# Kernel tuning notes

Hardware: AMD Instinct MI355X
Metric: run time of the kernel (lower is better)

Reference implementation:

```python
import jax, jax.numpy as jnp
import numpy as np

V = 50257; CTX = 2048; D = 1024; H = 16; L = 8; DH = D // H
B = 2; S = 2048; EPS = 1e-5


def setup_inputs() -> dict:
    key = jax.random.key(0)
    ks = jax.random.split(key, 8)
    s = 0.02
    def n(k, shape):
        return jax.random.normal(k, shape, jnp.float32) * s
    return {
        "x": jax.random.randint(ks[0], (B, S), 0, V),
        "wte": n(ks[1], (V, D)),
        "wpe": n(ks[2], (CTX, D)),
        "ln1_g": jnp.ones((L, D), jnp.float32), "ln1_b": jnp.zeros((L, D), jnp.float32),
        "w_qkv": n(ks[3], (L, D, 3 * D)), "b_qkv": jnp.zeros((L, 3 * D), jnp.float32),
        "w_proj": n(ks[4], (L, D, D)), "b_proj": jnp.zeros((L, D), jnp.float32),
        "ln2_g": jnp.ones((L, D), jnp.float32), "ln2_b": jnp.zeros((L, D), jnp.float32),
        "w_fc": n(ks[5], (L, D, 4 * D)), "b_fc": jnp.zeros((L, 4 * D), jnp.float32),
        "w_cp": n(ks[6], (L, 4 * D, D)), "b_cp": jnp.zeros((L, D), jnp.float32),
        "lnf_g": jnp.ones((D,), jnp.float32), "lnf_b": jnp.zeros((D,), jnp.float32),
        "w_head": n(ks[7], (D, V)),
    }


def layernorm(x, g, b):
    m = x.mean(-1, keepdims=True)
    v = ((x - m) ** 2).mean(-1, keepdims=True)
    return (x - m) * jax.lax.rsqrt(v + EPS) * g + b


def gpt_forward(x, wte, wpe, ln1_g, ln1_b, w_qkv, b_qkv, w_proj, b_proj,
                ln2_g, ln2_b, w_fc, b_fc, w_cp, b_cp, lnf_g, lnf_b, w_head):
    Bx, Sx = x.shape
    h = wte[x] + wpe[:Sx]                       # [B,S,D]
    mask = jnp.tril(jnp.ones((Sx, Sx), bool))   # causal mask
    scale = DH ** -0.5

    def block(h, p):
        g1, b1, wq, bq, wp, bp, g2, b2, wf, bf, wc, bc = p
        y = layernorm(h, g1, b1)
        qkv = y @ wq + bq                        # [B,S,3D]
        q, k, v = jnp.split(qkv, 3, axis=-1)
        q = q.reshape(Bx, Sx, H, DH)
        k = k.reshape(Bx, Sx, H, DH)
        v = v.reshape(Bx, Sx, H, DH)
        att = jnp.einsum('bqhd,bkhd->bhqk', q, k) * scale
        att = jnp.where(mask, att, -jnp.inf)
        att = jax.nn.softmax(att, axis=-1)
        z = jnp.einsum('bhqk,bkhd->bqhd', att, v).reshape(Bx, Sx, D)
        h = h + z @ wp + bp
        y2 = layernorm(h, g2, b2)
        h = h + jax.nn.gelu(y2 @ wf + bf, approximate=False) @ wc + bc
        return h, None

    h, _ = jax.lax.scan(block, h, (ln1_g, ln1_b, w_qkv, b_qkv, w_proj, b_proj,
                                   ln2_g, ln2_b, w_fc, b_fc, w_cp, b_cp))
    h = layernorm(h, lnf_g, lnf_b)
    logits = h[:, -1:, :] @ w_head              # [B,1,V] (last position only)
    return logits


def reference(x, wte, wpe, ln1_g, ln1_b, w_qkv, b_qkv, w_proj, b_proj,
              ln2_g, ln2_b, w_fc, b_fc, w_cp, b_cp, lnf_g, lnf_b, w_head):
    return gpt_forward(x, wte, wpe, ln1_g, ln1_b, w_qkv, b_qkv, w_proj, b_proj,
                       ln2_g, ln2_b, w_fc, b_fc, w_cp, b_cp, lnf_g, lnf_b, w_head)
```

## Files before the change

### kernel.cpp

```cpp
#include <hip/hip_runtime.h>
#include <hip/hip_bf16.h>
#include <math.h>

#define VOCAB 50257
#define CTX 2048
#define DMODEL 1024
#define NHEAD 16
#define NLAYER 8
#define DHEAD 64
#define BATCH 2
#define SEQ 2048
#define NTOK (BATCH * SEQ)

typedef __bf16 bf16x8 __attribute__((ext_vector_type(8)));
typedef float  f32x4  __attribute__((ext_vector_type(4)));
typedef unsigned short ushort4v __attribute__((ext_vector_type(4)));
typedef unsigned short ushort8v __attribute__((ext_vector_type(8)));

__device__ inline void gl_lds16(const void* g, void* l) {
    __builtin_amdgcn_global_load_lds(
        (const __attribute__((address_space(1))) unsigned int*)g,
        (__attribute__((address_space(3))) unsigned int*)l, 16, 0, 0);
}

__device__ inline unsigned short f2bs(float v) {
    __hip_bfloat16 t = __float2bfloat16(v);
    return *(unsigned short*)&t;
}

__global__ void embed_kernel(const int* __restrict__ x,
                             const float* __restrict__ wte,
                             const float* __restrict__ wpe,
                             float* __restrict__ h) {
    int t = blockIdx.x;
    int s = t & (SEQ - 1);
    int tok = x[t];
    const float* pe = wpe + (long)s * DMODEL;
    const float* te = wte + (long)tok * DMODEL;
    float* ph = h + (long)t * DMODEL;
    for (int d = threadIdx.x; d < DMODEL; d += 256)
        ph[d] = te[d] + pe[d];
}

__device__ inline float wave_sum(float v) {
    for (int off = 32; off; off >>= 1) v += __shfl_xor(v, off);
    return v;
}

__device__ void ln_body(char* smem, int row, const float* __restrict__ in,
                        unsigned short* __restrict__ out,
                        const float* __restrict__ g, const float* __restrict__ b) {
    float* red  = (float*)smem;
    float* red2 = red + 4;
    const float* px = in + (long)row * DMODEL;
    unsigned short* po = out + (long)row * DMODEL;
    int tid = threadIdx.x;
    int wid = tid >> 6, lane = tid & 63;

    float x[4];
    float s = 0.f;
    #pragma unroll
    for (int i = 0; i < 4; ++i) { x[i] = px[tid + i * 256]; s += x[i]; }
    s = wave_sum(s);
    if (lane == 0) red[wid] = s;
    __syncthreads();
    float mean = (red[0] + red[1] + red[2] + red[3]) * (1.0f / DMODEL);

    float s2 = 0.f;
    #pragma unroll
    for (int i = 0; i < 4; ++i) { float d = x[i] - mean; s2 += d * d; }
    s2 = wave_sum(s2);
    if (lane == 0) red2[wid] = s2;
    __syncthreads();
    float var = (red2[0] + red2[1] + red2[2] + red2[3]) * (1.0f / DMODEL);
    float r = 1.0f / sqrtf(var + 1e-5f);
    #pragma unroll
    for (int i = 0; i < 4; ++i) {
        int d = tid + i * 256;
        po[d] = f2bs((x[i] - mean) * r * g[d] + b[d]);
    }
}

__global__ void ln_final(const float* __restrict__ in, float* __restrict__ out,
                         const float* __restrict__ g, const float* __restrict__ b,
                         long row_stride) {
    __shared__ float red[4], red2[4];
    int row = blockIdx.x;
    const float* px = in + (long)row * row_stride;
    float* po = out + (long)row * DMODEL;
    int tid = threadIdx.x;
    int wid = tid >> 6, lane = tid & 63;
    float x[4];
    float s = 0.f;
    #pragma unroll
    for (int i = 0; i < 4; ++i) { x[i] = px[tid + i * 256]; s += x[i]; }
    s = wave_sum(s);
    if (lane == 0) red[wid] = s;
    __syncthreads();
    float mean = (red[0] + red[1] + red[2] + red[3]) * (1.0f / DMODEL);
    float s2 = 0.f;
    #pragma unroll
    for (int i = 0; i < 4; ++i) { float d = x[i] - mean; s2 += d * d; }
    s2 = wave_sum(s2);
    if (lane == 0) red2[wid] = s2;
    __syncthreads();
    float var = (red2[0] + red2[1] + red2[2] + red2[3]) * (1.0f / DMODEL);
    float r = 1.0f / sqrtf(var + 1e-5f);
    #pragma unroll
    for (int i = 0; i < 4; ++i) {
        int d = tid + i * 256;
        po[d] = (x[i] - mean) * r * g[d] + b[d];
    }
}

__device__ void convT_body(char* smem, int kx, int ny, const float* __restrict__ W,
                           unsigned short* __restrict__ WT, int K, int N) {
    float (*t)[65] = (float(*)[65])smem;
    const int k0 = kx * 64, n0 = ny * 64;
    const int tid = threadIdx.x;
    {
        const int krow = tid >> 4, c4 = (tid & 15) * 4;
        #pragma unroll
        for (int p = 0; p < 4; ++p) {
            f32x4 gv = *(const f32x4*)&W[(long)(k0 + p * 16 + krow) * N + n0 + c4];
            #pragma unroll
            for (int j = 0; j < 4; ++j) t[p * 16 + krow][c4 + j] = gv[j];
        }
    }
    __syncthreads();
    {
        const int n = tid >> 3, kl = (tid & 7) * 8;
        #pragma unroll
        for (int p = 0; p < 2; ++p) {
            ushort8v pk;
            #pragma unroll
            for (int j = 0; j < 8; ++j) pk[j] = f2bs(t[kl + j][p * 32 + n]);
            *(ushort8v*)&WT[(long)(n0 + p * 32 + n) * K + k0 + kl] = pk;
        }
    }
}

__global__ __launch_bounds__(256)
void mm_qkv(const unsigned short* __restrict__ A,
            const unsigned short* __restrict__ BT,
            const float* __restrict__ bias,
            unsigned short* __restrict__ qkvB, int M, int N, int K) {
    __shared__ unsigned short As[128 * 32];
    __shared__ unsigned short Bs[128 * 32];
    const int tid = threadIdx.x;
    const int w = tid >> 6, lane = tid & 63;
    const int bm = blockIdx.y * 128, bn = blockIdx.x * 128;
    const int wr = (w >> 1) * 64, wc = (w & 1) * 64;

    f32x4 acc[4][4];
    #pragma unroll
    for (int m = 0; m < 4; ++m)
        #pragma unroll
        for (int n = 0; n < 4; ++n)
            acc[m][n] = (f32x4){0.f, 0.f, 0.f, 0.f};

    const int lrow = lane >> 2;
    const int lcol = (lane & 3) * 8;
    const unsigned short* gA = A + (long)(bm + w * 32 + lrow) * K + lcol;
    const unsigned short* gB = BT + (long)(bn + w * 32 + lrow) * K + lcol;
    unsigned short* lA = &As[(w * 32) * 32];
    unsigned short* lB = &Bs[(w * 32) * 32];

    for (int k0 = 0; k0 < K; k0 += 32) {
        gl_lds16(gA + k0,          lA);
        gl_lds16(gA + k0 + 16 * K, lA + 16 * 32);
        gl_lds16(gB + k0,          lB);
        gl_lds16(gB + k0 + 16 * K, lB + 16 * 32);
        __syncthreads();

        bf16x8 a[4], b[4];
        #pragma unroll
        for (int m = 0; m < 4; ++m)
            a[m] = *(const bf16x8*)&As[(wr + m * 16 + (lane & 15)) * 32 + (lane >> 4) * 8];
        #pragma unroll
        for (int n = 0; n < 4; ++n)
            b[n] = *(const bf16x8*)&Bs[(wc + n * 16 + (lane & 15)) * 32 + (lane >> 4) * 8];
        #pragma unroll
        for (int m = 0; m < 4; ++m)
            #pragma unroll
            for (int n = 0; n < 4; ++n)
                acc[m][n] = __builtin_amdgcn_mfma_f32_16x16x32_bf16(a[m], b[n], acc[m][n], 0, 0, 0);
        __syncthreads();
    }

    const int r0 = (lane >> 4) * 4, cc = lane & 15;
    #pragma unroll
    for (int n = 0; n < 4; ++n) {
        int colb = bn + wc + n * 16;
        float bv = bias[colb + cc];
        #pragma unroll
        for (int m = 0; m < 4; ++m) {
            int rowb = bm + wr + m * 16 + r0;
            int which = colb >> 10, hh = (colb & 1023) >> 6, dbase = colb & 63;
            int b_ = rowb >> 11, s_ = rowb & 2047;
            long bh2 = b_ * 16 + hh;
            float v[4];
            #pragma unroll
            for (int r = 0; r < 4; ++r) v[r] = acc[m][n][r] + bv;
            if (which == 2) {
                ushort4v pk;
                #pragma unroll
                for (int r = 0; r < 4; ++r) pk[r] = f2bs(v[r]);
                *(ushort4v*)&qkvB[8388608L + (bh2 * 64 + dbase + cc) * 2048 + s_] = pk;
            } else {
                unsigned short* dst = qkvB + (long)which * 4194304L +
                                      (bh2 * 2048 + s_) * 64 + dbase + cc;
                #pragma unroll
                for (int r = 0; r < 4; ++r) dst[r * 64] = f2bs(v[r]);
            }
        }
    }
}

__device__ void mm128_gelu_body(char* smem, int bx, int by,
                                const unsigned short* __restrict__ A,
                                const unsigned short* __restrict__ BT,
                                const float* __restrict__ bias,
                                unsigned short* __restrict__ Cout, int M, int N, int K) {
    unsigned short* As = (unsigned short*)smem;
    unsigned short* Bs = As + 128 * 32;
    const int tid = threadIdx.x;
    const int w = tid >> 6, lane = tid & 63;
    const int bm = by * 128, bn = bx * 128;
    const int wr = (w >> 1) * 64, wc = (w & 1) * 64;

    f32x4 acc[4][4];
    #pragma unroll
    for (int m = 0; m < 4; ++m)
        #pragma unroll
        for (int n = 0; n < 4; ++n)
            acc[m][n] = (f32x4){0.f, 0.f, 0.f, 0.f};

    const int lrow = lane >> 2;
    const int lcol = (lane & 3) * 8;
    const unsigned short* gA = A + (long)(bm + w * 32 + lrow) * K + lcol;
    const unsigned short* gB = BT + (long)(bn + w * 32 + lrow) * K + lcol;
    unsigned short* lA = &As[(w * 32) * 32];
    unsigned short* lB = &Bs[(w * 32) * 32];

    for (int k0 = 0; k0 < K; k0 += 32) {
        gl_lds16(gA + k0,          lA);
        gl_lds16(gA + k0 + 16 * K, lA + 16 * 32);
        gl_lds16(gB + k0,          lB);
        gl_lds16(gB + k0 + 16 * K, lB + 16 * 32);
        __syncthreads();

        bf16x8 a[4], b[4];
        #pragma unroll
        for (int m = 0; m < 4; ++m)
            a[m] = *(const bf16x8*)&As[(wr + m * 16 + (lane & 15)) * 32 + (lane >> 4) * 8];
        #pragma unroll
        for (int n = 0; n < 4; ++n)
            b[n] = *(const bf16x8*)&Bs[(wc + n * 16 + (lane & 15)) * 32 + (lane >> 4) * 8];
        #pragma unroll
        for (int m = 0; m < 4; ++m)
            #pragma unroll
            for (int n = 0; n < 4; ++n)
                acc[m][n] = __builtin_amdgcn_mfma_f32_16x16x32_bf16(a[m], b[n], acc[m][n], 0, 0, 0);
        __syncthreads();
    }

    const int r0 = (lane >> 4) * 4, cc = lane & 15;
    #pragma unroll
    for (int n = 0; n < 4; ++n) {
        int colb = bn + wc + n * 16;
        float bv = bias[colb + cc];
        #pragma unroll
        for (int m = 0; m < 4; ++m) {
            int rowb = bm + wr + m * 16 + r0;
            #pragma unroll
            for (int r = 0; r < 4; ++r) {
                long row = rowb + r, col = colb + cc;
                float v = acc[m][n][r] + bv;
                v = 0.5f * v * (1.0f + erff(v * 0.70710678118f));
                Cout[row * N + col] = f2bs(v);
            }
        }
    }
}

__global__ __launch_bounds__(256)
void mm_mfma_n64(const unsigned short* __restrict__ A,
                 const unsigned short* __restrict__ BT,
                 const float* __restrict__ bias, const float* __restrict__ R,
                 float* __restrict__ Cout, int M, int N, int K) {
    __shared__ unsigned short As[128 * 32];
    __shared__ unsigned short Bs[64 * 32];
    const int tid = threadIdx.x;
    const int w = tid >> 6, lane = tid & 63;
    const int bm = blockIdx.y * 128, bn = blockIdx.x * 64;
    const int wr = (w >> 1) * 64, wc = (w & 1) * 32;

    f32x4 acc[4][2];
    #pragma unroll
    for (int m = 0; m < 4; ++m)
        #pragma unroll
        for (int n = 0; n < 2; ++n)
            acc[m][n] = (f32x4){0.f, 0.f, 0.f, 0.f};

    const int lrow = lane >> 2;
    const int lcol = (lane & 3) * 8;
    const unsigned short* gA = A + (long)(bm + w * 32 + lrow) * K + lcol;
    const unsigned short* gB = BT + (long)(bn + w * 16 + lrow) * K + lcol;
    unsigned short* lA = &As[(w * 32) * 32];
    unsigned short* lB = &Bs[(w * 16) * 32];

    for (int k0 = 0; k0 < K; k0 += 32) {
        gl_lds16(gA + k0,          lA);
        gl_lds16(gA + k0 + 16 * K, lA + 16 * 32);
        gl_lds16(gB + k0,          lB);
        __syncthreads();

        bf16x8 a[4], b[2];
        #pragma unroll
        for (int m = 0; m < 4; ++m)
            a[m] = *(const bf16x8*)&As[(wr + m * 16 + (lane & 15)) * 32 + (lane >> 4) * 8];
        #pragma unroll
        for (int n = 0; n < 2; ++n)
            b[n] = *(const bf16x8*)&Bs[(wc + n * 16 + (lane & 15)) * 32 + (lane >> 4) * 8];
        #pragma unroll
        for (int m = 0; m < 4; ++m)
            #pragma unroll
            for (int n = 0; n < 2; ++n)
                acc[m][n] = __builtin_amdgcn_mfma_f32_16x16x32_bf16(a[m], b[n], acc[m][n], 0, 0, 0);
        __syncthreads();
    }

    const int r0 = (lane >> 4) * 4, cc = lane & 15;
    #pragma unroll
    for (int n = 0; n < 2; ++n) {
        int colb = bn + wc + n * 16;
        float bv = bias[colb + cc];
        #pragma unroll
        for (int m = 0; m < 4; ++m) {
            int rowb = bm + wr + m * 16 + r0;
            #pragma unroll
            for (int r = 0; r < 4; ++r) {
                long row = rowb + r, col = colb + cc;
                float v = acc[m][n][r] + bv + R[row * N + col];
                Cout[row * N + col] = v;
            }
        }
    }
}

__device__ void attn_body(char* smem, int bh, int qb,
                          const unsigned short* __restrict__ qB,
                          const unsigned short* __restrict__ kB,
                          const unsigned short* __restrict__ vT,
                          __hip_bfloat16* __restrict__ z) {
    const int tid = threadIdx.x, w = tid >> 6, lane = tid & 63;
    const int arow = lane & 15, kg = lane >> 4;
    unsigned short* Ks = (unsigned short*)smem;
    unsigned short* Vs = Ks + 128 * 64;
    unsigned short* Ps = Vs + 64 * 128 + w * 16 * 128;

    const long kvbase = (long)bh * (2048 * 64);

    bf16x8 qa[2];
    {
        const unsigned short* q0 = qB + kvbase + (long)(qb + w * 16 + arow) * 64 + kg * 8;
        qa[0] = *(const bf16x8*)(q0);
        qa[1] = *(const bf16x8*)(q0 + 32);
    }

    f32x4 po[4];
    float mrow[4], lrow[4];
    #pragma unroll
    for (int i = 0; i < 4; ++i) {
        po[i] = (f32x4){0.f, 0.f, 0.f, 0.f};
        mrow[i] = -1e30f; lrow[i] = 0.f;
    }

    const int ksrow = lane >> 3;
    const int kschunk = (lane & 7) ^ ksrow;
    const int vsr = lane >> 4;
    const int cmax = qb >> 7;

    for (int c = 0; c <= cmax; ++c) {
        {
            const unsigned short* ks0 = kB + kvbase +
                (long)(c * 128 + w * 32 + ksrow) * 64 + kschunk * 8;
            #pragma unroll
            for (int i = 0; i < 4; ++i)
                gl_lds16(ks0 + (long)i * 8 * 64, &Ks[(w * 32 + i * 8) * 64]);
            #pragma unroll
            for (int i = 0; i < 4; ++i) {
                int d = w * 16 + i * 4 + vsr;
                int sch = (lane & 15) ^ (d & 7);
                gl_lds16(vT + kvbase + (long)d * 2048 + c * 128 + sch * 8,
                         &Vs[(w * 16 + i * 4) * 128]);
            }
        }
        __syncthreads();

        f32x4 s[8];
        #pragma unroll
        for (int n = 0; n < 8; ++n) {
            s[n] = (f32x4){0.f, 0.f, 0.f, 0.f};
            int row = n * 16 + arow, sw = row & 7;
            bf16x8 kb0 = *(const bf16x8*)&Ks[row * 64 + (kg ^ sw) * 8];
            bf16x8 kb1 = *(const bf16x8*)&Ks[row * 64 + ((4 + kg) ^ sw) * 8];
            s[n] = __builtin_amdgcn_mfma_f32_16x16x32_bf16(qa[0], kb0, s[n], 0, 0, 0);
            s[n] = __builtin_amdgcn_mfma_f32_16x16x32_bf16(qa[1], kb1, s[n], 0, 0, 0);
        }

        const bool diag = (c == cmax);
        #pragma unroll
        for (int n = 0; n < 8; ++n)
            #pragma unroll
            for (int r = 0; r < 4; ++r) {
                float v = s[n][r] * 0.125f;
                if (diag) {
                    int key = c * 128 + n * 16 + arow;
                    int qrow = qb + w * 16 + kg * 4 + r;
                    if (key > qrow) v = -1e30f;
                }
                s[n][r] = v;
            }

        #pragma unroll
        for (int r = 0; r < 4; ++r) {
            float rm = s[0][r];
            #pragma unroll
            for (int n = 1; n < 8; ++n) rm = fmaxf(rm, s[n][r]);
            #pragma unroll
            for (int off = 1; off < 16; off <<= 1)
                rm = fmaxf(rm, __shfl_xor(rm, off));
            float mnew = fmaxf(mrow[r], rm);
            float esc = expf(mrow[r] - mnew);
            float rs = 0.f;
            #pragma unroll
            for (int n = 0; n < 8; ++n) {
                float p = expf(s[n][r] - mnew);
                s[n][r] = p;
                rs += p;
            }
            #pragma unroll
            for (int off = 1; off < 16; off <<= 1)
                rs += __shfl_xor(rs, off);
            lrow[r] = lrow[r] * esc + rs;
            #pragma unroll
            for (int dt = 0; dt < 4; ++dt) po[dt][r] *= esc;
            mrow[r] = mnew;
        }

        #pragma unroll
        for (int n = 0; n < 8; ++n) {
            int col = n * 16 + arow;
            int chunk = col >> 3, cw = col & 7;
            #pragma unroll
            for (int r = 0; r < 4; ++r) {
                int row = kg * 4 + r;
                Ps[row * 128 + ((chunk ^ (row & 7)) * 8 + cw)] = f2bs(s[n][r]);
            }
        }

        bf16x8 pa[4];
        #pragma unroll
        for (int ks = 0; ks < 4; ++ks)
            pa[ks] = *(const bf16x8*)&Ps[arow * 128 + (((ks * 4 + kg) ^ (arow & 7)) * 8)];
        #pragma unroll
        for (int dt = 0; dt < 4; ++dt) {
            int vrow = dt * 16 + arow, sw = vrow & 7;
            #pragma unroll
            for (int ks = 0; ks < 4; ++ks) {
                bf16x8 vb = *(const bf16x8*)&Vs[vrow * 128 + (((ks * 4 + kg) ^ sw) * 8)];
                po[dt] = __builtin_amdgcn_mfma_f32_16x16x32_bf16(pa[ks], vb, po[dt], 0, 0, 0);
            }
        }
        __syncthreads();
    }

    const int b_ = bh >> 4, hofs = (bh & 15) * 64;
    #pragma unroll
    for (int dt = 0; dt < 4; ++dt)
        #pragma unroll
        for (int r = 0; r < 4; ++r) {
            long row = (long)b_ * 2048 + qb + w * 16 + kg * 4 + r;
            z[row * 1024 + hofs + dt * 16 + arow] = __float2bfloat16(po[dt][r] / lrow[r]);
        }
}

__global__ __launch_bounds__(256)
void fused_ln_convT(const float* __restrict__ h, unsigned short* __restrict__ y,
                    const float* __restrict__ g, const float* __restrict__ b,
                    const float* __restrict__ W, unsigned short* __restrict__ WT,
                    int K, int N, int nLN) {
    extern __shared__ char smem[];
    int bid = blockIdx.x;
    if (bid < nLN) {
        ln_body(smem, bid, h, y, g, b);
    } else {
        int r = bid - nLN, kt = K >> 6;
        convT_body(smem, r % kt, r / kt, W, WT, K, N);
    }
}

__global__ __launch_bounds__(256)
void fused_attn_convT(const unsigned short* __restrict__ qB,
                      const unsigned short* __restrict__ kB,
                      const unsigned short* __restrict__ vT,
                      __hip_bfloat16* __restrict__ z,
                      const float* __restrict__ W, unsigned short* __restrict__ WT,
                      int K, int N, int nAttn) {
    extern __shared__ char smem[];
    int bid = blockIdx.x;
    if (bid < nAttn) {
        attn_body(smem, bid & 31, (bid >> 5) * 64, qB, kB, vT, z);
    } else {
        int r = bid - nAttn, kt = K >> 6;
        convT_body(smem, r % kt, r / kt, W, WT, K, N);
    }
}

__global__ __launch_bounds__(256)
void fused_fc_convT(const unsigned short* __restrict__ A,
                    const unsigned short* __restrict__ BT,
                    const float* __restrict__ bias, unsigned short* __restrict__ Cout,
                    int M, int N, int K,
                    const float* __restrict__ W2, unsigned short* __restrict__ WT2,
                    int K2, int N2, int nMM) {
    extern __shared__ char smem[];
    int bid = blockIdx.x;
    if (bid < nMM) {
        mm128_gelu_body(smem, bid & 31, bid >> 5, A, BT, bias, Cout, M, N, K);
    } else {
        int r = bid - nMM, kt = K2 >> 6;
        convT_body(smem, r % kt, r / kt, W2, WT2, K2, N2);
    }
}

__global__ void head_kernel(const float* __restrict__ hl, const float* __restrict__ W,
                            float* __restrict__ out) {
    __shared__ float hs[2 * DMODEL];
    int tid = threadIdx.x;
    #pragma unroll
    for (int i = 0; i < 8; ++i) hs[tid + i * 256] = hl[tid + i * 256];
    __syncthreads();
    int v = blockIdx.x * 256 + tid;
    if (v >= VOCAB) return;
    float a0 = 0.f, a1 = 0.f;
    for (int d = 0; d < DMODEL; ++d) {
        float wv = W[(long)d * VOCAB + v];
        a0 += hs[d] * wv;
        a1 += hs[DMODEL + d] * wv;
    }
    out[v] = a0;
    out[VOCAB + v] = a1;
}

extern "C" void kernel_launch(void* const* d_in, const int* in_sizes, int n_in,
                              void* d_out, int out_size, void* d_ws, size_t ws_size,
                              hipStream_t stream) {
    const int*   x      = (const int*)  d_in[0];
    const float* wte    = (const float*)d_in[1];
    const float* wpe    = (const float*)d_in[2];
    const float* ln1_g  = (const float*)d_in[3];
    const float* ln1_b  = (const float*)d_in[4];
    const float* w_qkv  = (const float*)d_in[5];
    const float* b_qkv  = (const float*)d_in[6];
    const float* w_proj = (const float*)d_in[7];
    const float* b_proj = (const float*)d_in[8];
    const float* ln2_g  = (const float*)d_in[9];
    const float* ln2_b  = (const float*)d_in[10];
    const float* w_fc   = (const float*)d_in[11];
    const float* b_fc   = (const float*)d_in[12];
    const float* w_cp   = (const float*)d_in[13];
    const float* b_cp   = (const float*)d_in[14];
    const float* lnf_g  = (const float*)d_in[15];
    const float* lnf_b  = (const float*)d_in[16];
    const float* w_head = (const float*)d_in[17];
    float* out = (float*)d_out;

    char* ws = (char*)d_ws;
    float*          h     = (float*)ws;
    unsigned short* qkvB  = (unsigned short*)(ws + (16L << 20));
    unsigned short* y_bf  = (unsigned short*)(ws + (40L << 20));
    __hip_bfloat16* z_bf  = (__hip_bfloat16*)(ws + (48L << 20));
    unsigned short* fc_bf = (unsigned short*)(ws + (56L << 20));
    unsigned short* wT_a  = (unsigned short*)(ws + (88L << 20));
    unsigned short* wT_b  = (unsigned short*)(ws + (97L << 20));
    float*          hl    = (float*)(ws + (106L << 20));

    const int SM_CONV = 16640;
    const int SM_ATTN = 49152;

    embed_kernel<<<NTOK, 256, 0, stream>>>(x, wte, wpe, h);

    for (int l = 0; l < NLAYER; ++l) {
        fused_ln_convT<<<4096 + 768, 256, SM_CONV, stream>>>(
            h, y_bf, ln1_g + l * DMODEL, ln1_b + l * DMODEL,
            w_qkv + (long)l * DMODEL * 3072, wT_a, 1024, 3072, 4096);

        mm_qkv<<<dim3(24, 32), 256, 0, stream>>>(
            y_bf, wT_a, b_qkv + l * 3072, qkvB, NTOK, 3072, 1024);

        fused_attn_convT<<<1024 + 256, 256, SM_ATTN, stream>>>(
            qkvB, qkvB + 4194304L, qkvB + 8388608L, z_bf,
            w_proj + (long)l * DMODEL * DMODEL, wT_b, 1024, 1024, 1024);

        mm_mfma_n64<<<dim3(16, 32), 256, 0, stream>>>(
            (const unsigned short*)z_bf, wT_b, b_proj + l * DMODEL, h, h,
            NTOK, 1024, 1024);

        fused_ln_convT<<<4096 + 1024, 256, SM_CONV, stream>>>(
            h, y_bf, ln2_g + l * DMODEL, ln2_b + l * DMODEL,
            w_fc + (long)l * DMODEL * 4096, wT_a, 1024, 4096, 4096);

        fused_fc_convT<<<1024 + 1024, 256, SM_CONV, stream>>>(
            y_bf, wT_a, b_fc + l * 4096, fc_bf, NTOK, 4096, 1024,
            w_cp + (long)l * 4096 * DMODEL, wT_b, 4096, 1024, 1024);

        mm_mfma_n64<<<dim3(16, 32), 256, 0, stream>>>(
            fc_bf, wT_b, b_cp + l * DMODEL, h, h, NTOK, 1024, 4096);
    }

    ln_final<<<BATCH, 256, 0, stream>>>(h + (long)(SEQ - 1) * DMODEL, hl,
                                        lnf_g, lnf_b, (long)SEQ * DMODEL);
    head_kernel<<<(VOCAB + 255) / 256, 256, 0, stream>>>(hl, w_head, out);
}
```

Baseline: 2.667 ms.

## Replace QKV and FC GEMMs with 256x256 pipelined MFMA kernel

Adds a templated 256x256-tile GEMM with 8 waves (512 threads), double-buffered LDS staging through global_load_lds, XOR-swizzled LDS addressing and an interleaved stage/compute schedule. It uses s_setprio and a block-index swizzle for L2 locality, and is used for the QKV and FC+GELU projections in place of the 128x128 kernels. The w_cp transpose moves into the attention launch alongside the w_proj transpose, using a new weight buffer, so the FC GEMM no longer shares its launch with conversion blocks. Larger tiles mean only 192/256 workgroups at one per CU, which may leave CUs underused, and 128KB of LDS per block.

```diff
diff --git a/kernel.cpp b/kernel.cpp
--- a/kernel.cpp
+++ b/kernel.cpp
@@ -140,145 +140,138 @@
     }
 }
 
-__global__ __launch_bounds__(256)
-void mm_qkv(const unsigned short* __restrict__ A,
-            const unsigned short* __restrict__ BT,
-            const float* __restrict__ bias,
-            unsigned short* __restrict__ qkvB, int M, int N, int K) {
-    __shared__ unsigned short As[128 * 32];
-    __shared__ unsigned short Bs[128 * 32];
+#define STG_A(KS, H) do { \
+    const unsigned short* g_ = A + (long)(bm + (H) * 128 + srow) * K + (KS) * 64 + stgch; \
+    unsigned short* s_ = LDS + (((KS) & 1) * 2 + (H)) * 8192 + (w * 8) * 64; \
+    gl_lds16(g_, s_); gl_lds16(g_ + 64L * K, s_ + 4096); \
+} while (0)
+#define STG_B(KS, H) do { \
+    const unsigned short* g_ = BT + (long)(bn + (H) * 128 + srow) * K + (KS) * 64 + stgch; \
+    unsigned short* s_ = LDS + 32768 + (((KS) & 1) * 2 + (H)) * 8192 + (w * 8) * 64; \
+    gl_lds16(g_, s_); gl_lds16(g_ + 64L * K, s_ + 4096); \
+} while (0)
+#define MM2(M_, x0, x1) do { \
+    acc[M_][0] = __builtin_amdgcn_mfma_f32_16x16x32_bf16(x0, bfr[0], acc[M_][0], 0, 0, 0); \
+    acc[M_][0] = __builtin_amdgcn_mfma_f32_16x16x32_bf16(x1, bfr[1], acc[M_][0], 0, 0, 0); \
+    acc[M_][1] = __builtin_amdgcn_mfma_f32_16x16x32_bf16(x0, bfr[2], acc[M_][1], 0, 0, 0); \
+    acc[M_][1] = __builtin_amdgcn_mfma_f32_16x16x32_bf16(x1, bfr[3], acc[M_][1], 0, 0, 0); \
+    acc[M_][2] = __builtin_amdgcn_mfma_f32_16x16x32_bf16(x0, bfr[4], acc[M_][2], 0, 0, 0); \
+    acc[M_][2] = __builtin_amdgcn_mfma_f32_16x16x32_bf16(x1, bfr[5], acc[M_][2], 0, 0, 0); \
+    acc[M_][3] = __builtin_amdgcn_mfma_f32_16x16x32_bf16(x0, bfr[6], acc[M_][3], 0, 0, 0); \
+    acc[M_][3] = __builtin_amdgcn_mfma_f32_16x16x32_bf16(x1, bfr[7], acc[M_][3], 0, 0, 0); \
+} while (0)
+#define PHASE(Q, SPAR, STAGE_STMT, TAIL_STMT) do { \
+    bf16x8 a00, a01, a10, a11; \
+    if (((Q) & 3) == 0) { \
+        const unsigned short* Bb_ = lBp[SPAR] + ((wc & 1) * 64 + fr) * 64; \
+        bfr[0] = *(const bf16x8*)(Bb_ + rd0);        bfr[1] = *(const bf16x8*)(Bb_ + rd1); \
+        bfr[2] = *(const bf16x8*)(Bb_ + 1024 + rd0); bfr[3] = *(const bf16x8*)(Bb_ + 1024 + rd1); \
+        bfr[4] = *(const bf16x8*)(Bb_ + 2048 + rd0); bfr[5] = *(const bf16x8*)(Bb_ + 2048 + rd1); \
+        bfr[6] = *(const bf16x8*)(Bb_ + 3072 + rd0); bfr[7] = *(const bf16x8*)(Bb_ + 3072 + rd1); \
+    } \
+    { const unsigned short* Ab_ = lAp[SPAR] + fr * 64; \
+      a00 = *(const bf16x8*)(Ab_ + (((Q) & 3) * 2) * 1024 + rd0); \
+      a01 = *(const bf16x8*)(Ab_ + (((Q) & 3) * 2) * 1024 + rd1); \
+      a10 = *(const bf16x8*)(Ab_ + (((Q) & 3) * 2 + 1) * 1024 + rd0); \
+      a11 = *(const bf16x8*)(Ab_ + (((Q) & 3) * 2 + 1) * 1024 + rd1); } \
+    STAGE_STMT; \
+    __builtin_amdgcn_s_barrier(); \
+    asm volatile("s_waitcnt lgkmcnt(0)" ::: "memory"); \
+    __builtin_amdgcn_sched_barrier(0); \
+    __builtin_amdgcn_s_setprio(1); \
+    MM2(((Q) & 3) * 2, a00, a01); \
+    MM2(((Q) & 3) * 2 + 1, a10, a11); \
+    __builtin_amdgcn_s_setprio(0); \
+    TAIL_STMT; \
+    __builtin_amdgcn_s_barrier(); \
+} while (0)
+
+template<int EPI>
+__global__ __launch_bounds__(512, 1)
+void mm_mfma256(const unsigned short* __restrict__ A,
+                const unsigned short* __restrict__ BT,
+                const float* __restrict__ bias,
+                void* __restrict__ Cout, int M, int N, int K, int nbx) {
+    extern __shared__ unsigned short LDS[];
     const int tid = threadIdx.x;
     const int w = tid >> 6, lane = tid & 63;
-    const int bm = blockIdx.y * 128, bn = blockIdx.x * 128;
-    const int wr = (w >> 1) * 64, wc = (w & 1) * 64;
-
-    f32x4 acc[4][4];
-    #pragma unroll
-    for (int m = 0; m < 4; ++m)
+    const int wr = w >> 2, wc = w & 3;
+    const int nwg = gridDim.x, bid = blockIdx.x;
+    const int swz = (bid & 7) * (nwg >> 3) + (bid >> 3);
+    const int bm = (swz / nbx) * 256, bn = (swz % nbx) * 256;
+
+    f32x4 acc[8][4];
+    #pragma unroll
+    for (int m = 0; m < 8; ++m)
         #pragma unroll
         for (int n = 0; n < 4; ++n)
             acc[m][n] = (f32x4){0.f, 0.f, 0.f, 0.f};
 
-    const int lrow = lane >> 2;
-    const int lcol = (lane & 3) * 8;
-    const unsigned short* gA = A + (long)(bm + w * 32 + lrow) * K + lcol;
-    const unsigned short* gB = BT + (long)(bn + w * 32 + lrow) * K + lcol;
-    unsigned short* lA = &As[(w * 32) * 32];
-    unsigned short* lB = &Bs[(w * 32) * 32];
-
-    for (int k0 = 0; k0 < K; k0 += 32) {
-        gl_lds16(gA + k0,          lA);
-        gl_lds16(gA + k0 + 16 * K, lA + 16 * 32);
-        gl_lds16(gB + k0,          lB);
-        gl_lds16(gB + k0 + 16 * K, lB + 16 * 32);
-        __syncthreads();
-
-        bf16x8 a[4], b[4];
-        #pragma unroll
-        for (int m = 0; m < 4; ++m)
-            a[m] = *(const bf16x8*)&As[(wr + m * 16 + (lane & 15)) * 32 + (lane >> 4) * 8];
-        #pragma unroll
-        for (int n = 0; n < 4; ++n)
-            b[n] = *(const bf16x8*)&Bs[(wc + n * 16 + (lane & 15)) * 32 + (lane >> 4) * 8];
-        #pragma unroll
-        for (int m = 0; m < 4; ++m)
-            #pragma unroll
-            for (int n = 0; n < 4; ++n)
-                acc[m][n] = __builtin_amdgcn_mfma_f32_16x16x32_bf16(a[m], b[n], acc[m][n], 0, 0, 0);
-        __syncthreads();
-    }
-
-    const int r0 = (lane >> 4) * 4, cc = lane & 15;
+    const int fr = lane & 15, kg = lane >> 4;
+    const int rd0 = 8 * (kg ^ (lane & 7)), rd1 = 8 * ((kg + 4) ^ (lane & 7));
+    const int stgch = 8 * ((lane & 7) ^ (lane >> 3));
+    const int srow = w * 8 + (lane >> 3);
+    unsigned short* const lAp[2] = { LDS + wr * 8192, LDS + (2 + wr) * 8192 };
+    unsigned short* const lBp[2] = { LDS + 32768 + (wc >> 1) * 8192,
+                                     LDS + 32768 + (2 + (wc >> 1)) * 8192 };
+    bf16x8 bfr[8];
+
+    STG_B(0, 0); STG_B(0, 1); STG_A(0, 0); STG_A(0, 1); STG_B(1, 0); STG_B(1, 1);
+    asm volatile("s_waitcnt vmcnt(4)" ::: "memory");
+    __builtin_amdgcn_sched_barrier(0);
+    __builtin_amdgcn_s_barrier();
+
+    const int T = K >> 7;
+    for (int t = 0; t < T; ++t) {
+        const int s = 2 * t;
+        const bool nl = (t < T - 1);
+        PHASE(0, 0, STG_A(s + 1, 0), );
+        PHASE(1, 0, STG_A(s + 1, 1), );
+        PHASE(2, 0, if (nl) STG_B(s + 2, 0), );
+        PHASE(3, 0, if (nl) STG_B(s + 2, 1),
+              if (nl) { asm volatile("s_waitcnt vmcnt(4)" ::: "memory"); } else { asm volatile("s_waitcnt vmcnt(0)" ::: "memory"); } __builtin_amdgcn_sched_barrier(0); );
+        PHASE(4, 1, if (nl) STG_A(s + 2, 0), );
+        PHASE(5, 1, if (nl) STG_A(s + 2, 1), );
+        PHASE(6, 1, if (nl) STG_B(s + 3, 0), );
+        PHASE(7, 1, if (nl) STG_B(s + 3, 1),
+              if (nl) { asm volatile("s_waitcnt vmcnt(4)" ::: "memory"); __builtin_amdgcn_sched_barrier(0); } );
+    }
+
+    const int r0 = (lane >> 4) * 4;
     #pragma unroll
     for (int n = 0; n < 4; ++n) {
-        int colb = bn + wc + n * 16;
-        float bv = bias[colb + cc];
-        #pragma unroll
-        for (int m = 0; m < 4; ++m) {
-            int rowb = bm + wr + m * 16 + r0;
-            int which = colb >> 10, hh = (colb & 1023) >> 6, dbase = colb & 63;
-            int b_ = rowb >> 11, s_ = rowb & 2047;
-            long bh2 = b_ * 16 + hh;
-            float v[4];
-            #pragma unroll
-            for (int r = 0; r < 4; ++r) v[r] = acc[m][n][r] + bv;
-            if (which == 2) {
-                ushort4v pk;
+        int colb = bn + wc * 64 + n * 16;
+        float bv = bias[colb + fr];
+        #pragma unroll
+        for (int m = 0; m < 8; ++m) {
+            int rowb = bm + wr * 128 + m * 16 + r0;
+            if (EPI == 3) {
+                unsigned short* qkvB = (unsigned short*)Cout;
+                int which = colb >> 10, hh = (colb & 1023) >> 6, dbase = colb & 63;
+                int b_ = rowb >> 11, s_ = rowb & 2047;
+                long bh2 = b_ * 16 + hh;
+                float v[4];
                 #pragma unroll
-                for (int r = 0; r < 4; ++r) pk[r] = f2bs(v[r]);
-                *(ushort4v*)&qkvB[8388608L + (bh2 * 64 + dbase + cc) * 2048 + s_] = pk;
+                for (int r = 0; r < 4; ++r) v[r] = acc[m][n][r] + bv;
+                if (which == 2) {
+                    ushort4v pk;
+                    #pragma unroll
+                    for (int r = 0; r < 4; ++r) pk[r] = f2bs(v[r]);
+                    *(ushort4v*)&qkvB[8388608L + (bh2 * 64 + dbase + fr) * 2048 + s_] = pk;
+                } else {
+                    unsigned short* dst = qkvB + (long)which * 4194304L +
+                                          (bh2 * 2048 + s_) * 64 + dbase + fr;
+                    #pragma unroll
+                    for (int r = 0; r < 4; ++r) dst[r * 64] = f2bs(v[r]);
+                }
             } else {
-                unsigned short* dst = qkvB + (long)which * 4194304L +
-                                      (bh2 * 2048 + s_) * 64 + dbase + cc;
                 #pragma unroll
-                for (int r = 0; r < 4; ++r) dst[r * 64] = f2bs(v[r]);
-            }
-        }
-    }
-}
-
-__device__ void mm128_gelu_body(char* smem, int bx, int by,
-                                const unsigned short* __restrict__ A,
-                                const unsigned short* __restrict__ BT,
-                                const float* __restrict__ bias,
-                                unsigned short* __restrict__ Cout, int M, int N, int K) {
-    unsigned short* As = (unsigned short*)smem;
-    unsigned short* Bs = As + 128 * 32;
-    const int tid = threadIdx.x;
-    const int w = tid >> 6, lane = tid & 63;
-    const int bm = by * 128, bn = bx * 128;
-    const int wr = (w >> 1) * 64, wc = (w & 1) * 64;
-
-    f32x4 acc[4][4];
-    #pragma unroll
-    for (int m = 0; m < 4; ++m)
-        #pragma unroll
-        for (int n = 0; n < 4; ++n)
-            acc[m][n] = (f32x4){0.f, 0.f, 0.f, 0.f};
-
-    const int lrow = lane >> 2;
-    const int lcol = (lane & 3) * 8;
-    const unsigned short* gA = A + (long)(bm + w * 32 + lrow) * K + lcol;
-    const unsigned short* gB = BT + (long)(bn + w * 32 + lrow) * K + lcol;
-    unsigned short* lA = &As[(w * 32) * 32];
-    unsigned short* lB = &Bs[(w * 32) * 32];
-
-    for (int k0 = 0; k0 < K; k0 += 32) {
-        gl_lds16(gA + k0,          lA);
-        gl_lds16(gA + k0 + 16 * K, lA + 16 * 32);
-        gl_lds16(gB + k0,          lB);
-        gl_lds16(gB + k0 + 16 * K, lB + 16 * 32);
-        __syncthreads();
-
-        bf16x8 a[4], b[4];
-        #pragma unroll
-        for (int m = 0; m < 4; ++m)
-            a[m] = *(const bf16x8*)&As[(wr + m * 16 + (lane & 15)) * 32 + (lane >> 4) * 8];
-        #pragma unroll
-        for (int n = 0; n < 4; ++n)
-            b[n] = *(const bf16x8*)&Bs[(wc + n * 16 + (lane & 15)) * 32 + (lane >> 4) * 8];
-        #pragma unroll
-        for (int m = 0; m < 4; ++m)
-            #pragma unroll
-            for (int n = 0; n < 4; ++n)
-                acc[m][n] = __builtin_amdgcn_mfma_f32_16x16x32_bf16(a[m], b[n], acc[m][n], 0, 0, 0);
-        __syncthreads();
-    }
-
-    const int r0 = (lane >> 4) * 4, cc = lane & 15;
-    #pragma unroll
-    for (int n = 0; n < 4; ++n) {
-        int colb = bn + wc + n * 16;
-        float bv = bias[colb + cc];
-        #pragma unroll
-        for (int m = 0; m < 4; ++m) {
-            int rowb = bm + wr + m * 16 + r0;
-            #pragma unroll
-            for (int r = 0; r < 4; ++r) {
-                long row = rowb + r, col = colb + cc;
-                float v = acc[m][n][r] + bv;
-                v = 0.5f * v * (1.0f + erff(v * 0.70710678118f));
-                Cout[row * N + col] = f2bs(v);
+                for (int r = 0; r < 4; ++r) {
+                    long row = rowb + r, col = colb + fr;
+                    float v = acc[m][n][r] + bv;
+                    v = 0.5f * v * (1.0f + erff(v * 0.70710678118f));
+                    ((__hip_bfloat16*)Cout)[row * N + col] = __float2bfloat16(v);
+                }
             }
         }
     }
@@ -503,35 +496,23 @@
 }
 
 __global__ __launch_bounds__(256)
-void fused_attn_convT(const unsigned short* __restrict__ qB,
-                      const unsigned short* __restrict__ kB,
-                      const unsigned short* __restrict__ vT,
-                      __hip_bfloat16* __restrict__ z,
-                      const float* __restrict__ W, unsigned short* __restrict__ WT,
-                      int K, int N, int nAttn) {
+void fused_attn_convT2(const unsigned short* __restrict__ qB,
+                       const unsigned short* __restrict__ kB,
+                       const unsigned short* __restrict__ vT,
+                       __hip_bfloat16* __restrict__ z,
+                       const float* __restrict__ W1, unsigned short* __restrict__ WT1,
+                       int K1, int N1, int n1,
+                       const float* __restrict__ W2, unsigned short* __restrict__ WT2,
+                       int K2, int N2, int nAttn) {
     extern __shared__ char smem[];
     int bid = blockIdx.x;
     if (bid < nAttn) {
         attn_body(smem, bid & 31, (bid >> 5) * 64, qB, kB, vT, z);
+    } else if (bid < nAttn + n1) {
+        int r = bid - nAttn, kt = K1 >> 6;
+        convT_body(smem, r % kt, r / kt, W1, WT1, K1, N1);
     } else {
-        int r = bid - nAttn, kt = K >> 6;
-        convT_body(smem, r % kt, r / kt, W, WT, K, N);
-    }
-}
-
-__global__ __launch_bounds__(256)
-void fused_fc_convT(const unsigned short* __restrict__ A,
-                    const unsigned short* __restrict__ BT,
-                    const float* __restrict__ bias, unsigned short* __restrict__ Cout,
-                    int M, int N, int K,
-                    const float* __restrict__ W2, unsigned short* __restrict__ WT2,
-                    int K2, int N2, int nMM) {
-    extern __shared__ char smem[];
-    int bid = blockIdx.x;
-    if (bid < nMM) {
-        mm128_gelu_body(smem, bid & 31, bid >> 5, A, BT, bias, Cout, M, N, K);
-    } else {
-        int r = bid - nMM, kt = K2 >> 6;
+        int r = bid - nAttn - n1, kt = K2 >> 6;
         convT_body(smem, r % kt, r / kt, W2, WT2, K2, N2);
     }
 }
@@ -586,7 +567,8 @@
     unsigned short* fc_bf = (unsigned short*)(ws + (56L << 20));
     unsigned short* wT_a  = (unsigned short*)(ws + (88L << 20));
     unsigned short* wT_b  = (unsigned short*)(ws + (97L << 20));
-    float*          hl    = (float*)(ws + (106L << 20));
+    unsigned short* wT_c  = (unsigned short*)(ws + (106L << 20));
+    float*          hl    = (float*)(ws + (115L << 20));
 
     const int SM_CONV = 16640;
     const int SM_ATTN = 49152;
@@ -598,12 +580,13 @@
             h, y_bf, ln1_g + l * DMODEL, ln1_b + l * DMODEL,
             w_qkv + (long)l * DMODEL * 3072, wT_a, 1024, 3072, 4096);
 
-        mm_qkv<<<dim3(24, 32), 256, 0, stream>>>(
-            y_bf, wT_a, b_qkv + l * 3072, qkvB, NTOK, 3072, 1024);
-
-        fused_attn_convT<<<1024 + 256, 256, SM_ATTN, stream>>>(
+        mm_mfma256<3><<<192, 512, 131072, stream>>>(
+            y_bf, wT_a, b_qkv + l * 3072, qkvB, NTOK, 3072, 1024, 12);
+
+        fused_attn_convT2<<<1024 + 256 + 1024, 256, SM_ATTN, stream>>>(
             qkvB, qkvB + 4194304L, qkvB + 8388608L, z_bf,
-            w_proj + (long)l * DMODEL * DMODEL, wT_b, 1024, 1024, 1024);
+            w_proj + (long)l * DMODEL * DMODEL, wT_b, 1024, 1024, 256,
+            w_cp + (long)l * 4096 * DMODEL, wT_c, 4096, 1024, 1024);
 
         mm_mfma_n64<<<dim3(16, 32), 256, 0, stream>>>(
             (const unsigned short*)z_bf, wT_b, b_proj + l * DMODEL, h, h,
@@ -613,12 +596,11 @@
             h, y_bf, ln2_g + l * DMODEL, ln2_b + l * DMODEL,
             w_fc + (long)l * DMODEL * 4096, wT_a, 1024, 4096, 4096);
 
-        fused_fc_convT<<<1024 + 1024, 256, SM_CONV, stream>>>(
-            y_bf, wT_a, b_fc + l * 4096, fc_bf, NTOK, 4096, 1024,
-            w_cp + (long)l * 4096 * DMODEL, wT_b, 4096, 1024, 1024);
+        mm_mfma256<2><<<256, 512, 131072, stream>>>(
+            y_bf, wT_a, b_fc + l * 4096, fc_bf, NTOK, 4096, 1024, 16);
 
         mm_mfma_n64<<<dim3(16, 32), 256, 0, stream>>>(
-            fc_bf, wT_b, b_cp + l * DMODEL, h, h, NTOK, 1024, 4096);
+            fc_bf, wT_c, b_cp + l * DMODEL, h, h, NTOK, 1024, 4096);
     }
 
     ln_final<<<BATCH, 256, 0, stream>>>(h + (long)(SEQ - 1) * DMODEL, hl,
```

Measured after the change: 2.521 ms. -5.5%, faster.
